# Performance work log

Hardware: AMD Instinct MI355X
Metric: run time of the kernel (lower is better)

The kernel has to match this reference:

```python
import jax, jax.numpy as jnp
import numpy as np

N, E, H = 4096, 256, 8
DH = E // H
BS = 8
EPS = 1e-5


def setup_inputs() -> dict:
    key = jax.random.key(0)
    ks = jax.random.split(key, 12)
    xav = lambda k, shape: jax.random.uniform(k, shape, jnp.float32,
                                              -np.sqrt(6.0 / (shape[0] + shape[1])),
                                              np.sqrt(6.0 / (shape[0] + shape[1])))
    return {
        "x": jax.random.normal(ks[0], (N, E), jnp.float32),
        "pe": jax.random.normal(ks[1], (N, E), jnp.float32),
        "x_batch": jnp.sort(jax.random.randint(ks[2], (N,), 0, BS)).astype(jnp.int64),
        "Wq": xav(ks[3], (E, E)),
        "Wk": xav(ks[4], (E, E)),
        "Wv": xav(ks[5], (E, E)),
        "bq": jnp.zeros((E,), jnp.float32),
        "bk": jnp.zeros((E,), jnp.float32),
        "bv": jnp.zeros((E,), jnp.float32),
        "Wo": xav(ks[6], (E, E)),
        "bo": jnp.zeros((E,), jnp.float32),
        "gamma": jnp.ones((E,), jnp.float32),
        "beta": jnp.zeros((E,), jnp.float32),
    }


def reference(x, pe, x_batch, Wq, Wk, Wv, bq, bk, bv, Wo, bo, gamma, beta):
    # per-batch self-attention == global attention with block-diagonal mask
    xp = x + pe                                   # q and k get pos-embed, v does not
    q = (xp @ Wq.T + bq).reshape(N, H, DH)
    k = (xp @ Wk.T + bk).reshape(N, H, DH)
    v = (x @ Wv.T + bv).reshape(N, H, DH)
    scale = 1.0 / np.sqrt(DH)
    same = x_batch[:, None] == x_batch[None, :]   # [N, N] intra-batch mask
    scores = jnp.einsum('ihd,jhd->hij', q, k) * scale
    scores = jnp.where(same[None], scores, -jnp.inf)
    attn = jax.nn.softmax(scores, axis=-1)        # dropout=0 (eval)
    ctx = jnp.einsum('hij,jhd->ihd', attn, v).reshape(N, E)
    out = ctx @ Wo.T + bo
    y = out + x                                   # layer_drop=0; residual is v == x
    mu = jnp.mean(y, axis=-1, keepdims=True)
    var = jnp.mean((y - mu) ** 2, axis=-1, keepdims=True)
    return (y - mu) / jnp.sqrt(var + EPS) * gamma + beta
```

## Files before the change

### kernel.cpp

```cpp
#include <hip/hip_runtime.h>
#include <math.h>

namespace {

constexpr int N  = 4096;
constexpr int E  = 256;
constexpr int H  = 8;
constexpr int DH = 32;
constexpr int BS = 8;
constexpr float CL = 0.17677669529663687f * 1.4426950408889634f;

typedef __bf16 bf16x8 __attribute__((ext_vector_type(8)));
typedef __bf16 bf16x4 __attribute__((ext_vector_type(4)));
typedef float  f32x4  __attribute__((ext_vector_type(4)));

#if __has_builtin(__builtin_amdgcn_exp2f)
#define EXP2F(x) __builtin_amdgcn_exp2f(x)
#else
#define EXP2F(x) __expf((x) * 0.6931471805599453f)
#endif

__device__ inline bf16x8 pack8(float4 a, float4 b) {
  bf16x8 r;
  r[0] = (__bf16)a.x; r[1] = (__bf16)a.y; r[2] = (__bf16)a.z; r[3] = (__bf16)a.w;
  r[4] = (__bf16)b.x; r[5] = (__bf16)b.y; r[6] = (__bf16)b.z; r[7] = (__bf16)b.w;
  return r;
}


__global__ __launch_bounds__(256) void prep_kernel(
    const float* __restrict__ x, const float* __restrict__ pe,
    const int* __restrict__ xb,
    const float* __restrict__ Wq, const float* __restrict__ Wk,
    const float* __restrict__ Wv, const float* __restrict__ Wo,
    __bf16* __restrict__ xpef, __bf16* __restrict__ xvf,
    __bf16* __restrict__ wfrag, int* __restrict__ seg)
{
  const int bid  = blockIdx.x;
  const int wv4  = threadIdx.x >> 6;
  const int lane = threadIdx.x & 63;
  const int l15  = lane & 15, g = lane >> 4;

  if (bid < 512) {
    const int wid = bid * 4 + wv4;
    const int rt = wid >> 3, kt = wid & 7;
    const float* xr = x  + (size_t)(rt * 16 + l15) * E + kt * 32 + 8 * g;
    const float* pr = pe + (size_t)(rt * 16 + l15) * E + kt * 32 + 8 * g;
    float4 a0 = *(const float4*)xr;
    float4 a1 = *(const float4*)(xr + 4);
    const float4 p0 = *(const float4*)pr;
    const float4 p1 = *(const float4*)(pr + 4);
    *reinterpret_cast<bf16x8*>(xvf + (size_t)wid * 512 + lane * 8) = pack8(a0, a1);
    a0.x += p0.x; a0.y += p0.y; a0.z += p0.z; a0.w += p0.w;
    a1.x += p1.x; a1.y += p1.y; a1.z += p1.z; a1.w += p1.w;
    *reinterpret_cast<bf16x8*>(xpef + (size_t)wid * 512 + lane * 8) = pack8(a0, a1);
  } else if (bid < 640) {
    const int wid = (bid - 512) * 4 + wv4;
    const int mat = wid >> 7;
    const int rem = wid & 127;
    const int n16 = rem >> 3, kt = rem & 7;
    const float* __restrict__ W =
        (mat == 0) ? Wq : (mat == 1) ? Wk : (mat == 2) ? Wv : Wo;
    const float* wr = W + (size_t)(n16 * 16 + l15) * E + kt * 32 + 8 * g;
    *reinterpret_cast<bf16x8*>(wfrag + (size_t)wid * 512 + lane * 8) =
        pack8(*(const float4*)wr, *(const float4*)(wr + 4));
  } else {
    if (threadIdx.x <= BS) {
      const int t = threadIdx.x;
      int lo = 0, hi = N;
      while (lo < hi) { int mid = (lo + hi) >> 1; if (xb[mid] < t) lo = mid + 1; else hi = mid; }
      seg[t] = lo;
    }
  }
}

__global__ __launch_bounds__(256) void qkv_mfma(
    const __bf16* __restrict__ xpef, const __bf16* __restrict__ xvf,
    const __bf16* __restrict__ wfrag,
    const float* __restrict__ bq, const float* __restrict__ bk,
    const float* __restrict__ bv,
    __bf16* __restrict__ qfrag, __bf16* __restrict__ kfrag,
    __bf16* __restrict__ vfrag)
{
  const int mat  = blockIdx.y;
  const int rt   = blockIdx.x >> 1;
  const int half = blockIdx.x & 1;
  const int wv   = threadIdx.x >> 6;
  const int lane = threadIdx.x & 63;
  const int l15  = lane & 15, g = lane >> 4;
  const int m0   = rt * 16;
  const int cb0  = half * 128 + wv * 32;

  const __bf16* __restrict__ A = (mat < 2) ? xpef : xvf;
  const __bf16* __restrict__ W = wfrag + (size_t)mat * 65536;

  bf16x8 af[8];
#pragma unroll
  for (int kk = 0; kk < 8; ++kk)
    af[kk] = *reinterpret_cast<const bf16x8*>(A + (size_t)(rt * 8 + kk) * 512 + lane * 8);

  f32x4 acc0 = {0.f, 0.f, 0.f, 0.f};
  f32x4 acc1 = {0.f, 0.f, 0.f, 0.f};
  const int n16b = cb0 >> 4;
#pragma unroll
  for (int kk = 0; kk < 8; ++kk) {
    const bf16x8 wf0 = *reinterpret_cast<const bf16x8*>(
        W + (size_t)(n16b * 8 + kk) * 512 + lane * 8);
    const bf16x8 wf1 = *reinterpret_cast<const bf16x8*>(
        W + (size_t)((n16b + 1) * 8 + kk) * 512 + lane * 8);
    acc0 = __builtin_amdgcn_mfma_f32_16x16x32_bf16(wf0, af[kk], acc0, 0, 0, 0);
    acc1 = __builtin_amdgcn_mfma_f32_16x16x32_bf16(wf1, af[kk], acc1, 0, 0, 0);
  }

  const int token = m0 + l15;
  const f32x4 accs[2] = {acc0, acc1};

  if (mat < 2) {
    const float* __restrict__ bi = mat ? bk : bq;
    __bf16* __restrict__ dst = mat ? kfrag : qfrag;
#pragma unroll
    for (int nt = 0; nt < 2; ++nt) {
      const int e  = cb0 + nt * 16 + 4 * g;
      const float4 bb = *(const float4*)(bi + e);
      const int h  = e >> 5;
      const int gp = (e & 31) >> 3;
      const int ib = e & 7;
      bf16x4 o;
      o.x = (__bf16)(accs[nt][0] + bb.x);
      o.y = (__bf16)(accs[nt][1] + bb.y);
      o.z = (__bf16)(accs[nt][2] + bb.z);
      o.w = (__bf16)(accs[nt][3] + bb.w);
      size_t idx;
      if (mat == 0) {
        const int lp = (token & 15) + 16 * gp;
        idx = ((size_t)(h * 256 + rt) * 64 + lp) * 8 + ib;
      } else {
        const int t  = token >> 6, tk = token & 63;
        const int mt = 2 * (tk >> 5) + ((tk >> 2) & 1);
        const int lp = 4 * ((tk >> 3) & 3) + (tk & 3) + 16 * gp;
        idx = ((size_t)((h * 64 + t) * 4 + mt) * 64 + lp) * 8 + ib;
      }
      *reinterpret_cast<bf16x4*>(dst + idx) = o;
    }
  } else {
    const int t  = token >> 6, tk = token & 63;
    const int ks = (tk >> 5) & 1;
    const int gp = (tk >> 3) & 3;
    const int i  = tk & 7;
#pragma unroll
    for (int nt = 0; nt < 2; ++nt) {
      const int e0 = cb0 + nt * 16 + 4 * g;
      const float4 bb = *(const float4*)(bv + e0);
      const float bbr[4] = {bb.x, bb.y, bb.z, bb.w};
#pragma unroll
      for (int r = 0; r < 4; ++r) {
        const int d  = e0 + r;
        const int h  = d >> 5, dh = (d >> 4) & 1;
        const size_t idx =
            ((size_t)(((h * 64 + t) * 2 + ks) * 2 + dh) * 64 + (d & 15) + 16 * gp) * 8 + i;
        vfrag[idx] = (__bf16)(accs[nt][r] + bbr[r]);
      }
    }
  }
}

__global__ __launch_bounds__(512) void attn_proj_ln(
    const __bf16* __restrict__ qfrag, const __bf16* __restrict__ kfrag,
    const __bf16* __restrict__ vfrag, const int* __restrict__ xb,
    const int* __restrict__ seg,
    const float* __restrict__ x, const __bf16* __restrict__ wofrag,
    const float* __restrict__ bo, const float* __restrict__ gamma,
    const float* __restrict__ beta, float* __restrict__ out)
{
  const int rt   = blockIdx.x;
  const int m0   = rt * 16;
  const int h    = threadIdx.x >> 6;
  const int lane = threadIdx.x & 63;
  const int l15  = lane & 15;
  const int g    = lane >> 4;
  const int qrow = m0 + l15;

  __shared__ __bf16 cl[16][264];
  __shared__ float redS[8][16];
  __shared__ float redQ[8][16];

  {
    const int b  = xb[qrow];
    const int lo = seg[b];
    const int hi = seg[b + 1];

    const bf16x8 qf = *reinterpret_cast<const bf16x8*>(
        qfrag + (size_t)(h * 256 + rt) * 512 + lane * 8);

    const int kstart = __shfl(lo, 0, 64);
    const int kend   = __shfl(hi, 15, 64);

    f32x4 acc0 = {0.f, 0.f, 0.f, 0.f};
    f32x4 acc1 = {0.f, 0.f, 0.f, 0.f};
    float lsum = 0.f;

    for (int t = kstart >> 6; t * 64 < kend; ++t) {
      const int j0 = t * 64;
      const __bf16* kb4 = kfrag + (size_t)(h * 64 + t) * 2048 + lane * 8;
      const __bf16* vb4 = vfrag + (size_t)(h * 64 + t) * 2048 + lane * 8;

      const bf16x8 kf0 = *reinterpret_cast<const bf16x8*>(kb4);
      const bf16x8 kf1 = *reinterpret_cast<const bf16x8*>(kb4 + 512);
      const bf16x8 kf2 = *reinterpret_cast<const bf16x8*>(kb4 + 1024);
      const bf16x8 kf3 = *reinterpret_cast<const bf16x8*>(kb4 + 1536);
      const bf16x8 vf00 = *reinterpret_cast<const bf16x8*>(vb4);
      const bf16x8 vf01 = *reinterpret_cast<const bf16x8*>(vb4 + 512);
      const bf16x8 vf10 = *reinterpret_cast<const bf16x8*>(vb4 + 1024);
      const bf16x8 vf11 = *reinterpret_cast<const bf16x8*>(vb4 + 1536);

      const f32x4 z = {0.f, 0.f, 0.f, 0.f};
      f32x4 s[4];
      s[0] = __builtin_amdgcn_mfma_f32_16x16x32_bf16(kf0, qf, z, 0, 0, 0);
      s[1] = __builtin_amdgcn_mfma_f32_16x16x32_bf16(kf1, qf, z, 0, 0, 0);
      s[2] = __builtin_amdgcn_mfma_f32_16x16x32_bf16(kf2, qf, z, 0, 0, 0);
      s[3] = __builtin_amdgcn_mfma_f32_16x16x32_bf16(kf3, qf, z, 0, 0, 0);

      bf16x8 pa[2];
#pragma unroll
      for (int ks = 0; ks < 2; ++ks)
#pragma unroll
        for (int b_ = 0; b_ < 2; ++b_)
#pragma unroll
          for (int r = 0; r < 4; ++r) {
            const int key = j0 + 32 * ks + 8 * g + 4 * b_ + r;
            const float sc = s[2 * ks + b_][r] * CL;
            const float e  = (key >= lo && key < hi) ? EXP2F(sc) : 0.f;
            lsum += e;
            pa[ks][4 * b_ + r] = (__bf16)e;
          }

      acc0 = __builtin_amdgcn_mfma_f32_16x16x32_bf16(pa[0], vf00, acc0, 0, 0, 0);
      acc1 = __builtin_amdgcn_mfma_f32_16x16x32_bf16(pa[0], vf01, acc1, 0, 0, 0);
      acc0 = __builtin_amdgcn_mfma_f32_16x16x32_bf16(pa[1], vf10, acc0, 0, 0, 0);
      acc1 = __builtin_amdgcn_mfma_f32_16x16x32_bf16(pa[1], vf11, acc1, 0, 0, 0);
    }

    lsum += __shfl_xor(lsum, 16, 64);
    lsum += __shfl_xor(lsum, 32, 64);
    const float inv = 1.0f / lsum;
    float invr[4];
#pragma unroll
    for (int r = 0; r < 4; ++r) invr[r] = __shfl(inv, 4 * g + r, 64);

#pragma unroll
    for (int r = 0; r < 4; ++r) {
      cl[4 * g + r][h * DH + l15]      = (__bf16)(acc0[r] * invr[r]);
      cl[4 * g + r][h * DH + 16 + l15] = (__bf16)(acc1[r] * invr[r]);
    }
  }
  __syncthreads();

  {
    bf16x8 af[8];
#pragma unroll
    for (int kk = 0; kk < 8; ++kk)
      af[kk] = *reinterpret_cast<const bf16x8*>(&cl[l15][kk * 32 + 8 * g]);

    f32x4 acc[2];
    acc[0] = f32x4{0.f, 0.f, 0.f, 0.f};
    acc[1] = f32x4{0.f, 0.f, 0.f, 0.f};

#pragma unroll
    for (int kk = 0; kk < 8; ++kk)
#pragma unroll
      for (int nt = 0; nt < 2; ++nt) {
        const bf16x8 wf = *reinterpret_cast<const bf16x8*>(
            wofrag + (size_t)((h * 2 + nt) * 8 + kk) * 512 + lane * 8);
        acc[nt] = __builtin_amdgcn_mfma_f32_16x16x32_bf16(af[kk], wf, acc[nt], 0, 0, 0);
      }

    float yv[2][4];
    float s1[4], s2[4];
#pragma unroll
    for (int r = 0; r < 4; ++r) { s1[r] = 0.f; s2[r] = 0.f; }
#pragma unroll
    for (int nt = 0; nt < 2; ++nt) {
      const int c = h * 32 + nt * 16 + l15;
      const float bb = bo[c];
#pragma unroll
      for (int r = 0; r < 4; ++r) {
        const int row = m0 + 4 * g + r;
        const float y = acc[nt][r] + bb + x[(size_t)row * E + c];
        yv[nt][r] = y;
        s1[r] += y;
        s2[r] += y * y;
      }
    }
#pragma unroll
    for (int off = 1; off < 16; off <<= 1) {
#pragma unroll
      for (int r = 0; r < 4; ++r) {
        s1[r] += __shfl_xor(s1[r], off, 64);
        s2[r] += __shfl_xor(s2[r], off, 64);
      }
    }
    if (l15 == 0) {
#pragma unroll
      for (int r = 0; r < 4; ++r) {
        redS[h][4 * g + r] = s1[r];
        redQ[h][4 * g + r] = s2[r];
      }
    }
    __syncthreads();
    float mu[4], rs[4];
#pragma unroll
    for (int r = 0; r < 4; ++r) {
      float ts = 0.f, tq = 0.f;
#pragma unroll
      for (int w = 0; w < 8; ++w) { ts += redS[w][4 * g + r]; tq += redQ[w][4 * g + r]; }
      mu[r] = ts * (1.0f / E);
      const float var = tq * (1.0f / E) - mu[r] * mu[r];
      rs[r] = rsqrtf(var + 1e-5f);
    }
#pragma unroll
    for (int nt = 0; nt < 2; ++nt) {
      const int c = h * 32 + nt * 16 + l15;
      const float gg = gamma[c];
      const float bt = beta[c];
#pragma unroll
      for (int r = 0; r < 4; ++r) {
        const int row = m0 + 4 * g + r;
        out[(size_t)row * E + c] = (yv[nt][r] - mu[r]) * rs[r] * gg + bt;
      }
    }
  }
}

}

extern "C" void kernel_launch(void* const* d_in, const int* in_sizes, int n_in,
                              void* d_out, int out_size, void* d_ws, size_t ws_size,
                              hipStream_t stream) {
  const float* x     = (const float*)d_in[0];
  const float* pe    = (const float*)d_in[1];
  const int*   xb    = (const int*)d_in[2];
  const float* Wq    = (const float*)d_in[3];
  const float* Wk    = (const float*)d_in[4];
  const float* Wv    = (const float*)d_in[5];
  const float* bq    = (const float*)d_in[6];
  const float* bk    = (const float*)d_in[7];
  const float* bv    = (const float*)d_in[8];
  const float* Wo    = (const float*)d_in[9];
  const float* bo    = (const float*)d_in[10];
  const float* gamma = (const float*)d_in[11];
  const float* beta  = (const float*)d_in[12];
  float* out = (float*)d_out;

  __bf16* ws = (__bf16*)d_ws;
  const size_t NE = (size_t)N * E;
  __bf16* qfrag = ws;
  __bf16* kfrag = ws + NE;
  __bf16* vfrag = ws + 2 * NE;
  __bf16* xpef  = ws + 3 * NE;
  __bf16* xvf   = ws + 4 * NE;
  __bf16* wfrag = ws + 5 * NE;
  int*    seg   = (int*)(ws + 5 * NE + 4 * 65536);

  prep_kernel<<<dim3(641), 256, 0, stream>>>(x, pe, xb, Wq, Wk, Wv, Wo,
                                             xpef, xvf, wfrag, seg);
  qkv_mfma<<<dim3(512, 3), 256, 0, stream>>>(xpef, xvf, wfrag, bq, bk, bv,
                                             qfrag, kfrag, vfrag);
  attn_proj_ln<<<dim3(256), 512, 0, stream>>>(qfrag, kfrag, vfrag, xb, seg,
                                              x, wfrag + 3 * 65536,
                                              bo, gamma, beta, out);
}
```

Baseline: 38.03 us.

## Software-pipeline K/V tile loads in attention and W loads in QKV projection

The attention loop now double-buffers K and V fragments in two register sets, so the next 64-key tile is being fetched while the current tile's score MFMAs, exp and PV MFMAs run. MFMA sections are wrapped in s_setprio to raise wave priority around matrix work. The QKV projection kernel prefetches weight fragments two k-steps ahead through a small rotating register buffer. Together these aim to hide global load latency behind compute, at the cost of higher register pressure, which could lower occupancy.

```diff
diff --git a/kernel.cpp b/kernel.cpp
--- a/kernel.cpp
+++ b/kernel.cpp
@@ -102,14 +102,25 @@
   f32x4 acc0 = {0.f, 0.f, 0.f, 0.f};
   f32x4 acc1 = {0.f, 0.f, 0.f, 0.f};
   const int n16b = cb0 >> 4;
+  const __bf16* __restrict__ Wp0 = W + (size_t)(n16b * 8) * 512 + lane * 8;
+  const __bf16* __restrict__ Wp1 = W + (size_t)((n16b + 1) * 8) * 512 + lane * 8;
+
+  bf16x8 ww[4];
+  ww[0] = *reinterpret_cast<const bf16x8*>(Wp0);
+  ww[1] = *reinterpret_cast<const bf16x8*>(Wp1);
+  ww[2] = *reinterpret_cast<const bf16x8*>(Wp0 + 512);
+  ww[3] = *reinterpret_cast<const bf16x8*>(Wp1 + 512);
+
 #pragma unroll
   for (int kk = 0; kk < 8; ++kk) {
-    const bf16x8 wf0 = *reinterpret_cast<const bf16x8*>(
-        W + (size_t)(n16b * 8 + kk) * 512 + lane * 8);
-    const bf16x8 wf1 = *reinterpret_cast<const bf16x8*>(
-        W + (size_t)((n16b + 1) * 8 + kk) * 512 + lane * 8);
-    acc0 = __builtin_amdgcn_mfma_f32_16x16x32_bf16(wf0, af[kk], acc0, 0, 0, 0);
-    acc1 = __builtin_amdgcn_mfma_f32_16x16x32_bf16(wf1, af[kk], acc1, 0, 0, 0);
+    const bf16x8 cw0 = ww[(2 * kk) & 3];
+    const bf16x8 cw1 = ww[(2 * kk + 1) & 3];
+    if (kk < 6) {
+      ww[(2 * kk) & 3]     = *reinterpret_cast<const bf16x8*>(Wp0 + (size_t)(kk + 2) * 512);
+      ww[(2 * kk + 1) & 3] = *reinterpret_cast<const bf16x8*>(Wp1 + (size_t)(kk + 2) * 512);
+    }
+    acc0 = __builtin_amdgcn_mfma_f32_16x16x32_bf16(cw0, af[kk], acc0, 0, 0, 0);
+    acc1 = __builtin_amdgcn_mfma_f32_16x16x32_bf16(cw1, af[kk], acc1, 0, 0, 0);
   }
 
   const int token = m0 + l15;
@@ -164,6 +175,54 @@
   }
 }
 
+#define LOADT(S, T)                                                            \
+  {                                                                            \
+    const __bf16* kb4 = kfrag + (size_t)(h * 64 + (T)) * 2048 + lane * 8;      \
+    const __bf16* vb4 = vfrag + (size_t)(h * 64 + (T)) * 2048 + lane * 8;      \
+    k##S##0 = *reinterpret_cast<const bf16x8*>(kb4);                           \
+    k##S##1 = *reinterpret_cast<const bf16x8*>(kb4 + 512);                     \
+    k##S##2 = *reinterpret_cast<const bf16x8*>(kb4 + 1024);                    \
+    k##S##3 = *reinterpret_cast<const bf16x8*>(kb4 + 1536);                    \
+    v##S##0 = *reinterpret_cast<const bf16x8*>(vb4);                           \
+    v##S##1 = *reinterpret_cast<const bf16x8*>(vb4 + 512);                     \
+    v##S##2 = *reinterpret_cast<const bf16x8*>(vb4 + 1024);                    \
+    v##S##3 = *reinterpret_cast<const bf16x8*>(vb4 + 1536);                    \
+  }
+
+#define COMPUTE(S, T)                                                          \
+  {                                                                            \
+    const int j0c = (T) * 64;                                                  \
+    const f32x4 z = {0.f, 0.f, 0.f, 0.f};                                      \
+    __builtin_amdgcn_s_setprio(1);                                             \
+    const f32x4 s0 = __builtin_amdgcn_mfma_f32_16x16x32_bf16(k##S##0, qf, z, 0, 0, 0); \
+    const f32x4 s1 = __builtin_amdgcn_mfma_f32_16x16x32_bf16(k##S##1, qf, z, 0, 0, 0); \
+    const f32x4 s2 = __builtin_amdgcn_mfma_f32_16x16x32_bf16(k##S##2, qf, z, 0, 0, 0); \
+    const f32x4 s3 = __builtin_amdgcn_mfma_f32_16x16x32_bf16(k##S##3, qf, z, 0, 0, 0); \
+    __builtin_amdgcn_s_setprio(0);                                             \
+    bf16x8 pa0, pa1;                                                           \
+    _Pragma("unroll")                                                          \
+    for (int b_ = 0; b_ < 2; ++b_)                                             \
+      _Pragma("unroll")                                                        \
+      for (int r = 0; r < 4; ++r) {                                            \
+        const int key0 = j0c + 8 * g + 4 * b_ + r;                             \
+        const float e0 =                                                       \
+            (key0 >= lo && key0 < hi) ? EXP2F((b_ ? s1[r] : s0[r]) * CL) : 0.f;\
+        lsum += e0;                                                            \
+        pa0[4 * b_ + r] = (__bf16)e0;                                          \
+        const int key1 = key0 + 32;                                            \
+        const float e1 =                                                       \
+            (key1 >= lo && key1 < hi) ? EXP2F((b_ ? s3[r] : s2[r]) * CL) : 0.f;\
+        lsum += e1;                                                            \
+        pa1[4 * b_ + r] = (__bf16)e1;                                          \
+      }                                                                        \
+    __builtin_amdgcn_s_setprio(1);                                             \
+    acc0 = __builtin_amdgcn_mfma_f32_16x16x32_bf16(pa0, v##S##0, acc0, 0, 0, 0); \
+    acc1 = __builtin_amdgcn_mfma_f32_16x16x32_bf16(pa0, v##S##1, acc1, 0, 0, 0); \
+    acc0 = __builtin_amdgcn_mfma_f32_16x16x32_bf16(pa1, v##S##2, acc0, 0, 0, 0); \
+    acc1 = __builtin_amdgcn_mfma_f32_16x16x32_bf16(pa1, v##S##3, acc1, 0, 0, 0); \
+    __builtin_amdgcn_s_setprio(0);                                             \
+  }
+
 __global__ __launch_bounds__(512) void attn_proj_ln(
     const __bf16* __restrict__ qfrag, const __bf16* __restrict__ kfrag,
     const __bf16* __restrict__ vfrag, const int* __restrict__ xb,
@@ -194,50 +253,25 @@
 
     const int kstart = __shfl(lo, 0, 64);
     const int kend   = __shfl(hi, 15, 64);
+    const int t0 = kstart >> 6;
+    const int t1 = (kend + 63) >> 6;
 
     f32x4 acc0 = {0.f, 0.f, 0.f, 0.f};
     f32x4 acc1 = {0.f, 0.f, 0.f, 0.f};
     float lsum = 0.f;
 
-    for (int t = kstart >> 6; t * 64 < kend; ++t) {
-      const int j0 = t * 64;
-      const __bf16* kb4 = kfrag + (size_t)(h * 64 + t) * 2048 + lane * 8;
-      const __bf16* vb4 = vfrag + (size_t)(h * 64 + t) * 2048 + lane * 8;
-
-      const bf16x8 kf0 = *reinterpret_cast<const bf16x8*>(kb4);
-      const bf16x8 kf1 = *reinterpret_cast<const bf16x8*>(kb4 + 512);
-      const bf16x8 kf2 = *reinterpret_cast<const bf16x8*>(kb4 + 1024);
-      const bf16x8 kf3 = *reinterpret_cast<const bf16x8*>(kb4 + 1536);
-      const bf16x8 vf00 = *reinterpret_cast<const bf16x8*>(vb4);
-      const bf16x8 vf01 = *reinterpret_cast<const bf16x8*>(vb4 + 512);
-      const bf16x8 vf10 = *reinterpret_cast<const bf16x8*>(vb4 + 1024);
-      const bf16x8 vf11 = *reinterpret_cast<const bf16x8*>(vb4 + 1536);
-
-      const f32x4 z = {0.f, 0.f, 0.f, 0.f};
-      f32x4 s[4];
-      s[0] = __builtin_amdgcn_mfma_f32_16x16x32_bf16(kf0, qf, z, 0, 0, 0);
-      s[1] = __builtin_amdgcn_mfma_f32_16x16x32_bf16(kf1, qf, z, 0, 0, 0);
-      s[2] = __builtin_amdgcn_mfma_f32_16x16x32_bf16(kf2, qf, z, 0, 0, 0);
-      s[3] = __builtin_amdgcn_mfma_f32_16x16x32_bf16(kf3, qf, z, 0, 0, 0);
-
-      bf16x8 pa[2];
-#pragma unroll
-      for (int ks = 0; ks < 2; ++ks)
-#pragma unroll
-        for (int b_ = 0; b_ < 2; ++b_)
-#pragma unroll
-          for (int r = 0; r < 4; ++r) {
-            const int key = j0 + 32 * ks + 8 * g + 4 * b_ + r;
-            const float sc = s[2 * ks + b_][r] * CL;
-            const float e  = (key >= lo && key < hi) ? EXP2F(sc) : 0.f;
-            lsum += e;
-            pa[ks][4 * b_ + r] = (__bf16)e;
-          }
-
-      acc0 = __builtin_amdgcn_mfma_f32_16x16x32_bf16(pa[0], vf00, acc0, 0, 0, 0);
-      acc1 = __builtin_amdgcn_mfma_f32_16x16x32_bf16(pa[0], vf01, acc1, 0, 0, 0);
-      acc0 = __builtin_amdgcn_mfma_f32_16x16x32_bf16(pa[1], vf10, acc0, 0, 0, 0);
-      acc1 = __builtin_amdgcn_mfma_f32_16x16x32_bf16(pa[1], vf11, acc1, 0, 0, 0);
+    bf16x8 kA0, kA1, kA2, kA3, vA0, vA1, vA2, vA3;
+    bf16x8 kB0, kB1, kB2, kB3, vB0, vB1, vB2, vB3;
+
+    LOADT(A, t0)
+    for (int t = t0; t < t1; t += 2) {
+      const bool hasB = (t + 1 < t1);
+      if (hasB) LOADT(B, t + 1)
+      COMPUTE(A, t)
+      if (hasB) {
+        if (t + 2 < t1) LOADT(A, t + 2)
+        COMPUTE(B, t + 1)
+      }
     }
 
     lsum += __shfl_xor(lsum, 16, 64);
```

Result: slower. 39.70 us (+4.4%).

## Widen QKV blocks to full rows, software-pipeline weight loads, preload Wo fragments

Applied to the files above, without the earlier changes.

The QKV projection now has each block cover all 256 output columns of a 16-token tile (each wave does two 32-column passes), so the A fragments are loaded once per tile rather than twice and the grid is halved. Weight fragments are double-buffered in registers, prefetching two k-steps ahead of the MFMAs. In the attention kernel the Wo fragments are loaded into registers before the attention loop so their latency overlaps the attention work. The trade-off is fewer blocks for the QKV stage and higher register pressure in the attention kernel, which could lower occupancy.

```diff
diff --git a/kernel.cpp b/kernel.cpp
--- a/kernel.cpp
+++ b/kernel.cpp
@@ -83,13 +83,11 @@
     __bf16* __restrict__ vfrag)
 {
   const int mat  = blockIdx.y;
-  const int rt   = blockIdx.x >> 1;
-  const int half = blockIdx.x & 1;
+  const int rt   = blockIdx.x;
   const int wv   = threadIdx.x >> 6;
   const int lane = threadIdx.x & 63;
   const int l15  = lane & 15, g = lane >> 4;
   const int m0   = rt * 16;
-  const int cb0  = half * 128 + wv * 32;
 
   const __bf16* __restrict__ A = (mat < 2) ? xpef : xvf;
   const __bf16* __restrict__ W = wfrag + (size_t)mat * 65536;
@@ -99,66 +97,82 @@
   for (int kk = 0; kk < 8; ++kk)
     af[kk] = *reinterpret_cast<const bf16x8*>(A + (size_t)(rt * 8 + kk) * 512 + lane * 8);
 
-  f32x4 acc0 = {0.f, 0.f, 0.f, 0.f};
-  f32x4 acc1 = {0.f, 0.f, 0.f, 0.f};
-  const int n16b = cb0 >> 4;
-#pragma unroll
-  for (int kk = 0; kk < 8; ++kk) {
-    const bf16x8 wf0 = *reinterpret_cast<const bf16x8*>(
-        W + (size_t)(n16b * 8 + kk) * 512 + lane * 8);
-    const bf16x8 wf1 = *reinterpret_cast<const bf16x8*>(
-        W + (size_t)((n16b + 1) * 8 + kk) * 512 + lane * 8);
-    acc0 = __builtin_amdgcn_mfma_f32_16x16x32_bf16(wf0, af[kk], acc0, 0, 0, 0);
-    acc1 = __builtin_amdgcn_mfma_f32_16x16x32_bf16(wf1, af[kk], acc1, 0, 0, 0);
-  }
-
   const int token = m0 + l15;
-  const f32x4 accs[2] = {acc0, acc1};
-
-  if (mat < 2) {
-    const float* __restrict__ bi = mat ? bk : bq;
-    __bf16* __restrict__ dst = mat ? kfrag : qfrag;
-#pragma unroll
-    for (int nt = 0; nt < 2; ++nt) {
-      const int e  = cb0 + nt * 16 + 4 * g;
-      const float4 bb = *(const float4*)(bi + e);
-      const int h  = e >> 5;
-      const int gp = (e & 31) >> 3;
-      const int ib = e & 7;
-      bf16x4 o;
-      o.x = (__bf16)(accs[nt][0] + bb.x);
-      o.y = (__bf16)(accs[nt][1] + bb.y);
-      o.z = (__bf16)(accs[nt][2] + bb.z);
-      o.w = (__bf16)(accs[nt][3] + bb.w);
-      size_t idx;
-      if (mat == 0) {
-        const int lp = (token & 15) + 16 * gp;
-        idx = ((size_t)(h * 256 + rt) * 64 + lp) * 8 + ib;
-      } else {
-        const int t  = token >> 6, tk = token & 63;
-        const int mt = 2 * (tk >> 5) + ((tk >> 2) & 1);
-        const int lp = 4 * ((tk >> 3) & 3) + (tk & 3) + 16 * gp;
-        idx = ((size_t)((h * 64 + t) * 4 + mt) * 64 + lp) * 8 + ib;
-      }
-      *reinterpret_cast<bf16x4*>(dst + idx) = o;
-    }
-  } else {
-    const int t  = token >> 6, tk = token & 63;
-    const int ks = (tk >> 5) & 1;
-    const int gp = (tk >> 3) & 3;
-    const int i  = tk & 7;
-#pragma unroll
-    for (int nt = 0; nt < 2; ++nt) {
-      const int e0 = cb0 + nt * 16 + 4 * g;
-      const float4 bb = *(const float4*)(bv + e0);
-      const float bbr[4] = {bb.x, bb.y, bb.z, bb.w};
-#pragma unroll
-      for (int r = 0; r < 4; ++r) {
-        const int d  = e0 + r;
-        const int h  = d >> 5, dh = (d >> 4) & 1;
-        const size_t idx =
-            ((size_t)(((h * 64 + t) * 2 + ks) * 2 + dh) * 64 + (d & 15) + 16 * gp) * 8 + i;
-        vfrag[idx] = (__bf16)(accs[nt][r] + bbr[r]);
+
+#pragma unroll
+  for (int p = 0; p < 2; ++p) {
+    const int cb0  = wv * 64 + p * 32;
+    const int n16b = cb0 >> 4;
+    const __bf16* __restrict__ Wp0 = W + (size_t)(n16b * 8) * 512 + lane * 8;
+    const __bf16* __restrict__ Wp1 = W + (size_t)((n16b + 1) * 8) * 512 + lane * 8;
+
+    f32x4 acc0 = {0.f, 0.f, 0.f, 0.f};
+    f32x4 acc1 = {0.f, 0.f, 0.f, 0.f};
+
+    bf16x8 ww[4];
+    ww[0] = *reinterpret_cast<const bf16x8*>(Wp0);
+    ww[1] = *reinterpret_cast<const bf16x8*>(Wp1);
+    ww[2] = *reinterpret_cast<const bf16x8*>(Wp0 + 512);
+    ww[3] = *reinterpret_cast<const bf16x8*>(Wp1 + 512);
+
+#pragma unroll
+    for (int kk = 0; kk < 8; ++kk) {
+      const bf16x8 cw0 = ww[(2 * kk) & 3];
+      const bf16x8 cw1 = ww[(2 * kk + 1) & 3];
+      if (kk < 6) {
+        ww[(2 * kk) & 3]     = *reinterpret_cast<const bf16x8*>(Wp0 + (size_t)(kk + 2) * 512);
+        ww[(2 * kk + 1) & 3] = *reinterpret_cast<const bf16x8*>(Wp1 + (size_t)(kk + 2) * 512);
+      }
+      acc0 = __builtin_amdgcn_mfma_f32_16x16x32_bf16(cw0, af[kk], acc0, 0, 0, 0);
+      acc1 = __builtin_amdgcn_mfma_f32_16x16x32_bf16(cw1, af[kk], acc1, 0, 0, 0);
+    }
+
+    const f32x4 accs[2] = {acc0, acc1};
+    if (mat < 2) {
+      const float* __restrict__ bi = mat ? bk : bq;
+      __bf16* __restrict__ dst = mat ? kfrag : qfrag;
+#pragma unroll
+      for (int nt = 0; nt < 2; ++nt) {
+        const int e  = cb0 + nt * 16 + 4 * g;
+        const float4 bb = *(const float4*)(bi + e);
+        const int h  = e >> 5;
+        const int gp = (e & 31) >> 3;
+        const int ib = e & 7;
+        bf16x4 o;
+        o.x = (__bf16)(accs[nt][0] + bb.x);
+        o.y = (__bf16)(accs[nt][1] + bb.y);
+        o.z = (__bf16)(accs[nt][2] + bb.z);
+        o.w = (__bf16)(accs[nt][3] + bb.w);
+        size_t idx;
+        if (mat == 0) {
+          const int lp = (token & 15) + 16 * gp;
+          idx = ((size_t)(h * 256 + rt) * 64 + lp) * 8 + ib;
+        } else {
+          const int t  = token >> 6, tk = token & 63;
+          const int mt = 2 * (tk >> 5) + ((tk >> 2) & 1);
+          const int lp = 4 * ((tk >> 3) & 3) + (tk & 3) + 16 * gp;
+          idx = ((size_t)((h * 64 + t) * 4 + mt) * 64 + lp) * 8 + ib;
+        }
+        *reinterpret_cast<bf16x4*>(dst + idx) = o;
+      }
+    } else {
+      const int t  = token >> 6, tk = token & 63;
+      const int ks = (tk >> 5) & 1;
+      const int gp = (tk >> 3) & 3;
+      const int i  = tk & 7;
+#pragma unroll
+      for (int nt = 0; nt < 2; ++nt) {
+        const int e0 = cb0 + nt * 16 + 4 * g;
+        const float4 bb = *(const float4*)(bv + e0);
+        const float bbr[4] = {bb.x, bb.y, bb.z, bb.w};
+#pragma unroll
+        for (int r = 0; r < 4; ++r) {
+          const int d  = e0 + r;
+          const int h  = d >> 5, dh = (d >> 4) & 1;
+          const size_t idx =
+              ((size_t)(((h * 64 + t) * 2 + ks) * 2 + dh) * 64 + (d & 15) + 16 * gp) * 8 + i;
+          vfrag[idx] = (__bf16)(accs[nt][r] + bbr[r]);
+        }
       }
     }
   }
@@ -184,6 +198,14 @@
   __shared__ float redS[8][16];
   __shared__ float redQ[8][16];
 
+  bf16x8 wreg[2][8];
+#pragma unroll
+  for (int nt = 0; nt < 2; ++nt)
+#pragma unroll
+    for (int kk = 0; kk < 8; ++kk)
+      wreg[nt][kk] = *reinterpret_cast<const bf16x8*>(
+          wofrag + (size_t)((h * 2 + nt) * 8 + kk) * 512 + lane * 8);
+
   {
     const int b  = xb[qrow];
     const int lo = seg[b];
@@ -268,11 +290,9 @@
 #pragma unroll
     for (int kk = 0; kk < 8; ++kk)
 #pragma unroll
-      for (int nt = 0; nt < 2; ++nt) {
-        const bf16x8 wf = *reinterpret_cast<const bf16x8*>(
-            wofrag + (size_t)((h * 2 + nt) * 8 + kk) * 512 + lane * 8);
-        acc[nt] = __builtin_amdgcn_mfma_f32_16x16x32_bf16(af[kk], wf, acc[nt], 0, 0, 0);
-      }
+      for (int nt = 0; nt < 2; ++nt)
+        acc[nt] = __builtin_amdgcn_mfma_f32_16x16x32_bf16(af[kk], wreg[nt][kk],
+                                                          acc[nt], 0, 0, 0);
 
     float yv[2][4];
     float s1[4], s2[4];
@@ -363,7 +383,7 @@
 
   prep_kernel<<<dim3(641), 256, 0, stream>>>(x, pe, xb, Wq, Wk, Wv, Wo,
                                              xpef, xvf, wfrag, seg);
-  qkv_mfma<<<dim3(512, 3), 256, 0, stream>>>(xpef, xvf, wfrag, bq, bk, bv,
+  qkv_mfma<<<dim3(256, 3), 256, 0, stream>>>(xpef, xvf, wfrag, bq, bk, bv,
                                              qfrag, kfrag, vfrag);
   attn_proj_ln<<<dim3(256), 512, 0, stream>>>(qfrag, kfrag, vfrag, xb, seg,
                                               x, wfrag + 3 * 65536,
```

Result: slower. 38.82 us (+2.1%).
